# Optimization experiments

Measured on AMD Instinct MI355X. Metric: run time of the kernel, lower is better.

Reference implementation:

```python
import jax, jax.numpy as jnp
import numpy as np

H = 256      # hidden_dim
NH = 8       # num_heads
D = H // NH  # per-head dim
NEG = -(2.0**32) + 1.0
EPS = 1e-5


def setup_inputs() -> dict:
    key = jax.random.key(0)
    ks = jax.random.split(key, 12)
    N, Tq, Tk = 2, 2048, 2048
    s = 1.0 / np.sqrt(H)
    return {
        "Q": jax.random.normal(ks[0], (N, Tq, H), jnp.float32),
        "K": jax.random.normal(ks[1], (N, Tk, H), jnp.float32),
        "V": jax.random.normal(ks[2], (N, Tk, H), jnp.float32),
        "Wq": jax.random.normal(ks[3], (H, H), jnp.float32) * s,
        "bq": jnp.zeros((H,), jnp.float32),
        "Wk": jax.random.normal(ks[4], (H, H), jnp.float32) * s,
        "bk": jnp.zeros((H,), jnp.float32),
        "Wv": jax.random.normal(ks[5], (H, H), jnp.float32) * s,
        "bv": jnp.zeros((H,), jnp.float32),
        "gamma": jnp.ones((H,), jnp.float32),
        "beta": jnp.zeros((H,), jnp.float32),
    }


def _split_heads(x):
    # [N,T,H] -> [h,N,T,D]  (matches torch split(dim=2)+cat(dim=0): head-major)
    N, T, _ = x.shape
    return x.reshape(N, T, NH, D).transpose(2, 0, 1, 3)


def reference(Q, K, V, Wq, bq, Wk, bk, Wv, bv, gamma, beta):
    N, Tq, _ = Q.shape
    Tk = K.shape[1]
    Ql = jax.nn.relu(Q @ Wq + bq)
    Kl = jax.nn.relu(K @ Wk + bk)
    Vl = jax.nn.relu(V @ Wv + bv)
    Qh, Kh, Vh = _split_heads(Ql), _split_heads(Kl), _split_heads(Vl)

    scores = jnp.einsum("hnqd,hnkd->hnqk", Qh, Kh) / jnp.sqrt(jnp.float32(D))
    key_mask = jnp.sign(jnp.abs(K).sum(-1))    # [N,Tk]
    scores = jnp.where(key_mask[None, :, None, :] == 0, NEG, scores)
    attn = jax.nn.softmax(scores / 0.01, axis=-1)
    query_mask = jnp.sign(jnp.abs(Q).sum(-1))  # [N,Tq]
    attn = attn * query_mask[None, :, :, None]  # dropout p=0 -> identity

    ctx = jnp.einsum("hnqk,hnkd->hnqd", attn[..., :-1], Vh[:, :, :-1, :])
    out = ctx.transpose(1, 2, 0, 3).reshape(N, Tq, H)

    mu = out.mean(-1, keepdims=True)
    var = ((out - mu) ** 2).mean(-1, keepdims=True)
    out = (out - mu) / jnp.sqrt(var + EPS) * gamma + beta

    weight = attn.transpose(1, 2, 0, 3).reshape(N, Tq, NH * Tk).mean(-1)
    return out, weight
```

## Files before the change

kernel.cpp:

```cpp
#include <hip/hip_runtime.h>
#include <math.h>

#define H_DIM 256
#define NHEAD 8
#define DHEAD 32
#define NB 2
#define TSEQ 2048
#define LN_EPS 1e-5f

#define QK2_SCALE 25.503486f
#define SPLIT 4
#define TILES_PER (TSEQ / 64 / SPLIT)

typedef _Float16 half8 __attribute__((ext_vector_type(8)));
typedef _Float16 half4t __attribute__((ext_vector_type(4)));
typedef _Float16 half2t __attribute__((ext_vector_type(2)));
typedef float f32x4 __attribute__((ext_vector_type(4)));

__device__ __forceinline__ f32x4 mfma16(half8 a, half8 b, f32x4 c) {
  return __builtin_amdgcn_mfma_f32_16x16x32_f16(a, b, c, 0, 0, 0);
}
__device__ __forceinline__ float exp2fast(float x) {
  return __builtin_amdgcn_exp2f(x);
}
__device__ __forceinline__ half2t pkrtz(float a, float b) {
  return __builtin_bit_cast(half2t, __builtin_amdgcn_cvt_pkrtz(a, b));
}

#define GLOAD_LDS(gp, lp)                                            \
  __builtin_amdgcn_global_load_lds(                                  \
      (const __attribute__((address_space(1))) void*)(gp),           \
      (__attribute__((address_space(3))) void*)(lp), 16, 0, 0)

__global__ __launch_bounds__(256) void pack_mask_kernel(
    const float* __restrict__ K,
    const float* __restrict__ Wq, const float* __restrict__ Wk, const float* __restrict__ Wv,
    float* __restrict__ kmask,
    half8* __restrict__ WpkHi, half8* __restrict__ WpkLo) {
  const int tid = threadIdx.x;
  if (blockIdx.x < 1024) {
    const int wid = tid >> 6, lane = tid & 63;
    int row = blockIdx.x * 4 + wid;
    const float* src = K + (size_t)row * H_DIM;
    float4 v = *(const float4*)(src + lane * 4);
    float s = fabsf(v.x) + fabsf(v.y) + fabsf(v.z) + fabsf(v.w);
    #pragma unroll
    for (int off = 32; off > 0; off >>= 1) s += __shfl_xor(s, off);
    if (lane == 0) kmask[row] = (s != 0.0f) ? 1.0f : 0.0f;
    return;
  }
  int slot = (blockIdx.x - 1024) * 256 + tid;
  int lane = slot & 63;
  int fg = (slot >> 6) & 15;
  int s  = (slot >> 10) & 7;
  int which = slot >> 13;
  const float* W = which == 0 ? Wq : which == 1 ? Wk : Wv;
  int j  = fg * 16 + (lane & 15);
  int kb = s * 32 + (lane >> 4) * 8;
  half8 hi, lo;
  #pragma unroll
  for (int jj = 0; jj < 8; ++jj) {
    float x = W[(size_t)(kb + jj) * H_DIM + j];
    _Float16 h = (_Float16)x;
    hi[jj] = h;
    lo[jj] = (_Float16)(x - (float)h);
  }
  WpkHi[slot] = hi;
  WpkLo[slot] = lo;
}

__global__ __launch_bounds__(256, 3) void proj_kernel(
    const float* __restrict__ Q, const float* __restrict__ K, const float* __restrict__ V,
    const float* __restrict__ bq, const float* __restrict__ bk, const float* __restrict__ bv,
    const half8* __restrict__ WpkHi, const half8* __restrict__ WpkLo,
    const float* __restrict__ kmask,
    half8* __restrict__ Gqhi, half8* __restrict__ Gqlo,
    half8* __restrict__ Gkhi, half8* __restrict__ Gklo, half8* __restrict__ Gv,
    half8* __restrict__ AmaskF, float* __restrict__ qmask) {
  const int which = blockIdx.z;
  const float* X    = which == 0 ? Q  : which == 1 ? K  : V;
  const float* bias = which == 0 ? bq : which == 1 ? bk : bv;

  __shared__ __align__(16) float T[64 * 68];

  const int tid = threadIdx.x;
  const int w = tid >> 6, lane = tid & 63;
  const int l15 = lane & 15, quad = lane >> 4;
  const int mbase = blockIdx.y * 64;
  const int nfg   = blockIdx.x * 4;
  const int nn   = mbase >> 11;
  const int tile = blockIdx.y & 31;

  half8 ahi[8], alo[8];
  {
    const bool doqm = (which == 0) && (blockIdx.x == 0);
    float sabs = 0.0f;
    const float* xrow = X + (size_t)(mbase + w * 16 + l15) * H_DIM + quad * 8;
    #pragma unroll
    for (int s = 0; s < 8; ++s) {
      float4 a0 = *(const float4*)(xrow + s * 32);
      float4 a1 = *(const float4*)(xrow + s * 32 + 4);
      float xs[8] = {a0.x, a0.y, a0.z, a0.w, a1.x, a1.y, a1.z, a1.w};
      if (doqm) {
        #pragma unroll
        for (int i = 0; i < 8; ++i) sabs += fabsf(xs[i]);
      }
      #pragma unroll
      for (int i = 0; i < 8; ++i) {
        _Float16 h = (_Float16)xs[i];
        ahi[s][i] = h;
        alo[s][i] = (_Float16)(xs[i] - (float)h);
      }
    }
    if (doqm) {
      sabs += __shfl_xor(sabs, 16);
      sabs += __shfl_xor(sabs, 32);
      if (quad == 0) qmask[mbase + w * 16 + l15] = (sabs != 0.0f) ? 1.0f : 0.0f;
    }
  }

  f32x4 acc[4];
  #pragma unroll
  for (int f = 0; f < 4; ++f) acc[f] = (f32x4){0.f, 0.f, 0.f, 0.f};

  #pragma unroll
  for (int s = 0; s < 8; ++s) {
    const half8* ph = WpkHi + (((size_t)which * 8 + s) * 16 + nfg) * 64 + lane;
    const half8* pl = WpkLo + (((size_t)which * 8 + s) * 16 + nfg) * 64 + lane;
    #pragma unroll
    for (int f = 0; f < 4; ++f) {
      half8 BH = ph[f * 64];
      half8 BL = pl[f * 64];
      acc[f] = mfma16(ahi[s], BH, acc[f]);
      acc[f] = mfma16(ahi[s], BL, acc[f]);
      acc[f] = mfma16(alo[s], BH, acc[f]);
    }
  }

  #pragma unroll
  for (int f = 0; f < 4; ++f) {
    float bj = bias[blockIdx.x * 64 + f * 16 + l15];
    #pragma unroll
    for (int r = 0; r < 4; ++r) {
      int row = w * 16 + quad * 4 + r;
      float val = fmaxf(acc[f][r] + bj, 0.0f);
      if (which == 2 && ((mbase + row) & (TSEQ - 1)) == TSEQ - 1) val = 0.0f;
      T[row * 68 + f * 16 + l15] = val;
    }
  }
  __syncthreads();

  if (which < 2) {
    const int fq = tid >> 6, lp = tid & 63;
    const int kdc = lp >> 4, krlo = lp & 15;
    const int row = fq * 16 + krlo;
    const float sc = (which == 0) ? QK2_SCALE : 1.0f;
    #pragma unroll
    for (int hs = 0; hs < 2; ++hs) {
      const float* p = &T[row * 68 + hs * 32 + kdc * 8];
      float4 a0 = *(const float4*)p;
      float4 a1 = *(const float4*)(p + 4);
      float xs[8] = {a0.x, a0.y, a0.z, a0.w, a1.x, a1.y, a1.z, a1.w};
      half8 hi, lo;
      #pragma unroll
      for (int i = 0; i < 8; ++i) {
        float x = xs[i] * sc;
        _Float16 h = (_Float16)x;
        hi[i] = h;
        lo[i] = (_Float16)(x - (float)h);
      }
      int hn = (blockIdx.x * 2 + hs) * NB + nn;
      size_t di = ((size_t)hn * 32 + tile) * 256 + tid;
      if (which == 0) { Gqhi[di] = hi; Gqlo[di] = lo; }
      else            { Gkhi[di] = hi; Gklo[di] = lo; }
    }
    if (which == 1 && blockIdx.x == 0 && tid < 128) {
      int c = tid >> 6, lane2 = tid & 63;
      int quad2 = lane2 >> 4, l15b = lane2 & 15;
      half8 am;
      #pragma unroll
      for (int j = 0; j < 8; ++j)
        am[j] = (l15b == 0) ? (_Float16)kmask[(size_t)nn * TSEQ + tile * 64 + c * 32 + quad2 * 8 + j]
                            : (_Float16)0.0f;
      AmaskF[(((size_t)nn * 32 + tile) * 2 + c) * 64 + lane2] = am;
    }
  } else {
    const int top = tid >> 6, mid = (tid >> 4) & 3, low = tid & 15;
    const int c = top >> 1, hh = top & 1;
    const int trow0 = (c * 4 + mid) * 8;
    float km[8];
    #pragma unroll
    for (int j = 0; j < 8; ++j)
      km[j] = kmask[(size_t)nn * TSEQ + tile * 64 + trow0 + j];
    #pragma unroll
    for (int hs = 0; hs < 2; ++hs) {
      const int col = hs * 32 + hh * 16 + low;
      half8 v8;
      #pragma unroll
      for (int j = 0; j < 8; ++j)
        v8[j] = (_Float16)(T[(trow0 + j) * 68 + col] * km[j]);
      int hn = (blockIdx.x * 2 + hs) * NB + nn;
      Gv[((size_t)hn * 32 + tile) * 256 + tid] = v8;
    }
  }
}

__global__ __launch_bounds__(256, 4) void attn_kernel(
    const half8* __restrict__ Gqhi, const half8* __restrict__ Gqlo,
    const half8* __restrict__ Gkhi, const half8* __restrict__ Gklo,
    const half8* __restrict__ Gv, const half8* __restrict__ AmaskF,
    _Float16* __restrict__ Opf, float* __restrict__ Mp, float* __restrict__ Lp) {
  __shared__ __align__(16) half8 KhB[2][256];
  __shared__ __align__(16) half8 KlB[2][256];
  __shared__ __align__(16) half8 VB[2][256];
  __shared__ __align__(16) half8 AB[2][128];
  __shared__ __align__(16) _Float16 Pbuf[4][16][72];

  const int tid = threadIdx.x;
  const int w = tid >> 6, lane = tid & 63;
  const int l15 = lane & 15, quad = lane >> 4;

  const int b = blockIdx.x;
  const int g    = ((b & 7) << 1) | ((b >> 3) & 1);
  const int qt   = (b >> 4) & 15;
  const int sblk = b >> 8;
  const int n = g & 1;

  const size_t fbase = (size_t)g * 32 * 256;
  const int tile0 = sblk * TILES_PER;

  const size_t qoff = fbase + (size_t)(qt * 2) * 256 + w * 64 + lane;
  half8 qhiA = Gqhi[qoff];
  half8 qloA = Gqlo[qoff];
  half8 qhiB = Gqhi[qoff + 256];
  half8 qloB = Gqlo[qoff + 256];

  float mA = -1.0e30f, mB = -1.0e30f;
  f32x4 O0A = {0.f,0.f,0.f,0.f}, O1A = O0A, OlA = O0A;
  f32x4 O0B = O0A, O1B = O0A, OlB = O0A;

  const half8* gkh = Gkhi + fbase + (size_t)tile0 * 256;
  const half8* gkl = Gklo + fbase + (size_t)tile0 * 256;
  const half8* gvv = Gv   + fbase + (size_t)tile0 * 256;
  const half8* gam = AmaskF + (size_t)(n * 32 + tile0) * 128;

  GLOAD_LDS(gkh + tid, &KhB[0][tid]);
  GLOAD_LDS(gkl + tid, &KlB[0][tid]);
  GLOAD_LDS(gvv + tid, &VB[0][tid]);
  if (tid < 128) GLOAD_LDS(gam + tid, &AB[0][tid]);
  __syncthreads();

  #pragma unroll
  for (int tt = 0; tt < TILES_PER; ++tt) {
    const int cur = tt & 1, nxt = cur ^ 1;
    if (tt < TILES_PER - 1) {
      GLOAD_LDS(gkh + (tt + 1) * 256 + tid, &KhB[nxt][tid]);
      GLOAD_LDS(gkl + (tt + 1) * 256 + tid, &KlB[nxt][tid]);
      GLOAD_LDS(gvv + (tt + 1) * 256 + tid, &VB[nxt][tid]);
      if (tid < 128) GLOAD_LDS(gam + (tt + 1) * 128 + tid, &AB[nxt][tid]);
    }

    f32x4 SA[4], SB[4];
    #pragma unroll
    for (int f = 0; f < 4; ++f) {
      half8 KH = KhB[cur][f * 64 + lane];
      half8 KL = KlB[cur][f * 64 + lane];
      f32x4 a = (f32x4){0.f, 0.f, 0.f, 0.f};
      a = mfma16(KL, qhiA, a);
      a = mfma16(KH, qloA, a);
      a = mfma16(KH, qhiA, a);
      SA[f] = a;
      f32x4 bb = (f32x4){0.f, 0.f, 0.f, 0.f};
      bb = mfma16(KL, qhiB, bb);
      bb = mfma16(KH, qloB, bb);
      bb = mfma16(KH, qhiB, bb);
      SB[f] = bb;
    }

    half8 am0 = AB[cur][lane];
    half8 am1 = AB[cur][64 + lane];
    const half8* vbuf = (const half8*)VB[cur];

#define SM_PV(S, m_q, O0, O1, Ol)                                              \
    {                                                                          \
      float t0 = fmaxf(fmaxf(S[0][0], S[0][1]), fmaxf(S[0][2], S[0][3]));      \
      float t1 = fmaxf(fmaxf(S[1][0], S[1][1]), fmaxf(S[1][2], S[1][3]));      \
      float t2 = fmaxf(fmaxf(S[2][0], S[2][1]), fmaxf(S[2][2], S[2][3]));      \
      float t3 = fmaxf(fmaxf(S[3][0], S[3][1]), fmaxf(S[3][2], S[3][3]));      \
      float mx = fmaxf(fmaxf(t0, t1), fmaxf(t2, t3));                          \
      mx = fmaxf(mx, __shfl_xor(mx, 16));                                      \
      mx = fmaxf(mx, __shfl_xor(mx, 32));                                      \
      float mnew = fmaxf(m_q, mx);                                             \
      float alpha = exp2fast(m_q - mnew);                                      \
      m_q = mnew;                                                              \
      _Pragma("unroll")                                                        \
      for (int f = 0; f < 4; ++f) {                                            \
        float p0 = exp2fast(S[f][0] - m_q);                                    \
        float p1 = exp2fast(S[f][1] - m_q);                                    \
        float p2 = exp2fast(S[f][2] - m_q);                                    \
        float p3 = exp2fast(S[f][3] - m_q);                                    \
        half2t a01 = pkrtz(p0, p1);                                            \
        half2t a23 = pkrtz(p2, p3);                                            \
        half4t pk4;                                                            \
        pk4[0] = a01[0]; pk4[1] = a01[1]; pk4[2] = a23[0]; pk4[3] = a23[1];    \
        *(half4t*)&Pbuf[w][l15][f * 16 + quad * 4] = pk4;                      \
      }                                                                        \
      _Pragma("unroll")                                                        \
      for (int r = 0; r < 4; ++r) { O0[r] *= alpha; O1[r] *= alpha; }          \
      Ol[0] *= alpha;                                                          \
      asm volatile("s_waitcnt lgkmcnt(0)" ::: "memory");                       \
      _Pragma("unroll")                                                        \
      for (int c = 0; c < 2; ++c) {                                            \
        half8 pb = *(const half8*)&Pbuf[w][l15][c * 32 + quad * 8];            \
        O0 = mfma16(vbuf[(c * 2 + 0) * 64 + lane], pb, O0);                    \
        O1 = mfma16(vbuf[(c * 2 + 1) * 64 + lane], pb, O1);                    \
        Ol = mfma16(c == 0 ? am0 : am1, pb, Ol);                               \
      }                                                                        \
    }

    SM_PV(SA, mA, O0A, O1A, OlA)
    SM_PV(SB, mB, O0B, O1B, OlB)
#undef SM_PV

    __syncthreads();
  }

  {
    int qA = qt * 128 + w * 16 + l15;
    size_t rowbase = (size_t)(sblk * 16 + g) * TSEQ;
    size_t idxA = (rowbase + qA) * DHEAD;
    size_t idxB = (rowbase + qA + 64) * DHEAD;
    half4t o0A = {(_Float16)O0A[0], (_Float16)O0A[1], (_Float16)O0A[2], (_Float16)O0A[3]};
    half4t o1A = {(_Float16)O1A[0], (_Float16)O1A[1], (_Float16)O1A[2], (_Float16)O1A[3]};
    half4t o0B = {(_Float16)O0B[0], (_Float16)O0B[1], (_Float16)O0B[2], (_Float16)O0B[3]};
    half4t o1B = {(_Float16)O1B[0], (_Float16)O1B[1], (_Float16)O1B[2], (_Float16)O1B[3]};
    *(half4t*)&Opf[idxA + quad * 4]      = o0A;
    *(half4t*)&Opf[idxA + 16 + quad * 4] = o1A;
    *(half4t*)&Opf[idxB + quad * 4]      = o0B;
    *(half4t*)&Opf[idxB + 16 + quad * 4] = o1B;
    if (quad == 0) {
      Mp[rowbase + qA]      = mA;
      Lp[rowbase + qA]      = OlA[0];
      Mp[rowbase + qA + 64] = mB;
      Lp[rowbase + qA + 64] = OlB[0];
    }
  }
}

__global__ __launch_bounds__(256) void ln_kernel(
    const _Float16* __restrict__ Opf, const float* __restrict__ Mp, const float* __restrict__ Lp,
    const float* __restrict__ gamma, const float* __restrict__ beta,
    const float* __restrict__ qmask,
    float* __restrict__ out, float* __restrict__ wout) {
  const int wid = threadIdx.x >> 6, lane = threadIdx.x & 63;
  const int row = blockIdx.x * 4 + wid;
  const int n = row >> 11, q = row & (TSEQ - 1);
  const int hh = lane >> 3;
  const int hn = hh * NB + n;
  const int dbase = (lane & 7) * 4;

  float m[SPLIT], l[SPLIT];
  half4t P[SPLIT];
  #pragma unroll
  for (int i = 0; i < SPLIT; ++i) {
    size_t si = (size_t)(i * 16 + hn) * TSEQ + q;
    P[i] = *(const half4t*)&Opf[si * DHEAD + dbase];
    m[i] = Mp[si];
    l[i] = Lp[si];
  }
  float mm = m[0];
  #pragma unroll
  for (int i = 1; i < SPLIT; ++i) mm = fmaxf(mm, m[i]);
  float denom = 0.f;
  float a[SPLIT];
  #pragma unroll
  for (int i = 0; i < SPLIT; ++i) { a[i] = exp2fast(m[i] - mm); denom += l[i] * a[i]; }
  float qm = qmask[row];
  float inv = qm / denom;

  float4 x = make_float4(0.f, 0.f, 0.f, 0.f);
  #pragma unroll
  for (int i = 0; i < SPLIT; ++i) {
    x.x += (float)P[i][0] * a[i]; x.y += (float)P[i][1] * a[i];
    x.z += (float)P[i][2] * a[i]; x.w += (float)P[i][3] * a[i];
  }
  x.x *= inv; x.y *= inv; x.z *= inv; x.w *= inv;

  float s = x.x + x.y + x.z + x.w;
  #pragma unroll
  for (int off = 32; off > 0; off >>= 1) s += __shfl_xor(s, off);
  float mu = s * (1.0f / H_DIM);
  float dx0 = x.x - mu, dx1 = x.y - mu, dx2 = x.z - mu, dx3 = x.w - mu;
  float sq = dx0 * dx0 + dx1 * dx1 + dx2 * dx2 + dx3 * dx3;
  #pragma unroll
  for (int off = 32; off > 0; off >>= 1) sq += __shfl_xor(sq, off);
  float rstd = rsqrtf(sq * (1.0f / H_DIM) + LN_EPS);
  float4 g = *(const float4*)(gamma + lane * 4);
  float4 bb = *(const float4*)(beta + lane * 4);
  float4 y;
  y.x = dx0 * rstd * g.x + bb.x;
  y.y = dx1 * rstd * g.y + bb.y;
  y.z = dx2 * rstd * g.z + bb.z;
  y.w = dx3 * rstd * g.w + bb.w;
  *(float4*)(out + (size_t)row * H_DIM + lane * 4) = y;
  if (lane == 0) wout[row] = qm * (1.0f / TSEQ);
}

extern "C" void kernel_launch(void* const* d_in, const int* in_sizes, int n_in,
                              void* d_out, int out_size, void* d_ws, size_t ws_size,
                              hipStream_t stream) {
  const float* Q  = (const float*)d_in[0];
  const float* K  = (const float*)d_in[1];
  const float* V  = (const float*)d_in[2];
  const float* Wq = (const float*)d_in[3];
  const float* bq = (const float*)d_in[4];
  const float* Wk = (const float*)d_in[5];
  const float* bk = (const float*)d_in[6];
  const float* Wv = (const float*)d_in[7];
  const float* bv = (const float*)d_in[8];
  const float* gamma = (const float*)d_in[9];
  const float* beta  = (const float*)d_in[10];

  char* ws = (char*)d_ws;
  const size_t NFRAG = (size_t)16 * 32 * 256;
  _Float16* Opf = (_Float16*)ws;
  half8* Gqhi = (half8*)(ws + (size_t)SPLIT * 16 * TSEQ * DHEAD * 2);
  half8* Gqlo = Gqhi + NFRAG;
  half8* Gkhi = Gqlo + NFRAG;
  half8* Gklo = Gkhi + NFRAG;
  half8* Gv   = Gklo + NFRAG;
  float* Mp = (float*)(Gv + NFRAG);
  float* Lp = Mp + SPLIT * 16 * TSEQ;
  float* qmask = Lp + SPLIT * 16 * TSEQ;
  float* kmask = qmask + NB * TSEQ;
  half8* WpkHi = (half8*)(kmask + NB * TSEQ);
  half8* WpkLo = WpkHi + 24576;
  half8* AmaskF = WpkLo + 24576;

  float* out  = (float*)d_out;
  float* wout = out + (size_t)NB * TSEQ * H_DIM;

  hipLaunchKernelGGL(pack_mask_kernel, dim3(1024 + 96), dim3(256), 0, stream,
                     K, Wq, Wk, Wv, kmask, WpkHi, WpkLo);
  hipLaunchKernelGGL(proj_kernel, dim3(H_DIM / 64, NB * TSEQ / 64, 3), dim3(256), 0, stream,
                     Q, K, V, bq, bk, bv, WpkHi, WpkLo, kmask,
                     Gqhi, Gqlo, Gkhi, Gklo, Gv, AmaskF, qmask);
  hipLaunchKernelGGL(attn_kernel, dim3(16 * 16 * SPLIT), dim3(256), 0, stream,
                     Gqhi, Gqlo, Gkhi, Gklo, Gv, AmaskF, Opf, Mp, Lp);
  hipLaunchKernelGGL(ln_kernel, dim3(NB * TSEQ / 4), dim3(256), 0, stream,
                     Opf, Mp, Lp, gamma, beta, qmask, out, wout);
}
```

Before: 124.4 us.

## Remove pack/mask kernel; split weights inline and apply key mask in attention

Drops the separate weight-packing and key-mask kernel. The projection kernel now reads fp32 weights directly and splits them into fp16 hi/lo parts on the fly, and it computes the key mask alongside the query mask. The attention kernel loads a per-tile fp32 key mask into shared memory and multiplies it into the softmax probabilities, replacing the precomputed mask fragments with a constant ones vector for the row-sum. This saves one launch and the intermediate buffers. In exchange, the projection kernel does strided scalar weight loads and repeated conversions in every block, and the attention inner loop gains extra multiplies and shared-memory reads.

```diff
diff --git a/kernel.cpp b/kernel.cpp
--- a/kernel.cpp
+++ b/kernel.cpp
@@ -32,53 +32,16 @@
       (const __attribute__((address_space(1))) void*)(gp),           \
       (__attribute__((address_space(3))) void*)(lp), 16, 0, 0)
 
-__global__ __launch_bounds__(256) void pack_mask_kernel(
-    const float* __restrict__ K,
-    const float* __restrict__ Wq, const float* __restrict__ Wk, const float* __restrict__ Wv,
-    float* __restrict__ kmask,
-    half8* __restrict__ WpkHi, half8* __restrict__ WpkLo) {
-  const int tid = threadIdx.x;
-  if (blockIdx.x < 1024) {
-    const int wid = tid >> 6, lane = tid & 63;
-    int row = blockIdx.x * 4 + wid;
-    const float* src = K + (size_t)row * H_DIM;
-    float4 v = *(const float4*)(src + lane * 4);
-    float s = fabsf(v.x) + fabsf(v.y) + fabsf(v.z) + fabsf(v.w);
-    #pragma unroll
-    for (int off = 32; off > 0; off >>= 1) s += __shfl_xor(s, off);
-    if (lane == 0) kmask[row] = (s != 0.0f) ? 1.0f : 0.0f;
-    return;
-  }
-  int slot = (blockIdx.x - 1024) * 256 + tid;
-  int lane = slot & 63;
-  int fg = (slot >> 6) & 15;
-  int s  = (slot >> 10) & 7;
-  int which = slot >> 13;
-  const float* W = which == 0 ? Wq : which == 1 ? Wk : Wv;
-  int j  = fg * 16 + (lane & 15);
-  int kb = s * 32 + (lane >> 4) * 8;
-  half8 hi, lo;
-  #pragma unroll
-  for (int jj = 0; jj < 8; ++jj) {
-    float x = W[(size_t)(kb + jj) * H_DIM + j];
-    _Float16 h = (_Float16)x;
-    hi[jj] = h;
-    lo[jj] = (_Float16)(x - (float)h);
-  }
-  WpkHi[slot] = hi;
-  WpkLo[slot] = lo;
-}
-
 __global__ __launch_bounds__(256, 3) void proj_kernel(
     const float* __restrict__ Q, const float* __restrict__ K, const float* __restrict__ V,
+    const float* __restrict__ Wq, const float* __restrict__ Wk, const float* __restrict__ Wv,
     const float* __restrict__ bq, const float* __restrict__ bk, const float* __restrict__ bv,
-    const half8* __restrict__ WpkHi, const half8* __restrict__ WpkLo,
-    const float* __restrict__ kmask,
     half8* __restrict__ Gqhi, half8* __restrict__ Gqlo,
     half8* __restrict__ Gkhi, half8* __restrict__ Gklo, half8* __restrict__ Gv,
-    half8* __restrict__ AmaskF, float* __restrict__ qmask) {
+    float* __restrict__ qmask, float* __restrict__ kmask) {
   const int which = blockIdx.z;
   const float* X    = which == 0 ? Q  : which == 1 ? K  : V;
+  const float* Wsel = which == 0 ? Wq : which == 1 ? Wk : Wv;
   const float* bias = which == 0 ? bq : which == 1 ? bk : bv;
 
   __shared__ __align__(16) float T[64 * 68];
@@ -93,7 +56,7 @@
 
   half8 ahi[8], alo[8];
   {
-    const bool doqm = (which == 0) && (blockIdx.x == 0);
+    const bool domask = (blockIdx.x == 0) && (which < 2);
     float sabs = 0.0f;
     const float* xrow = X + (size_t)(mbase + w * 16 + l15) * H_DIM + quad * 8;
     #pragma unroll
@@ -101,7 +64,7 @@
       float4 a0 = *(const float4*)(xrow + s * 32);
       float4 a1 = *(const float4*)(xrow + s * 32 + 4);
       float xs[8] = {a0.x, a0.y, a0.z, a0.w, a1.x, a1.y, a1.z, a1.w};
-      if (doqm) {
+      if (domask) {
         #pragma unroll
         for (int i = 0; i < 8; ++i) sabs += fabsf(xs[i]);
       }
@@ -112,10 +75,11 @@
         alo[s][i] = (_Float16)(xs[i] - (float)h);
       }
     }
-    if (doqm) {
+    if (domask) {
       sabs += __shfl_xor(sabs, 16);
       sabs += __shfl_xor(sabs, 32);
-      if (quad == 0) qmask[mbase + w * 16 + l15] = (sabs != 0.0f) ? 1.0f : 0.0f;
+      float* dst = (which == 0) ? qmask : kmask;
+      if (quad == 0) dst[mbase + w * 16 + l15] = (sabs != 0.0f) ? 1.0f : 0.0f;
     }
   }
 
@@ -125,12 +89,17 @@
 
   #pragma unroll
   for (int s = 0; s < 8; ++s) {
-    const half8* ph = WpkHi + (((size_t)which * 8 + s) * 16 + nfg) * 64 + lane;
-    const half8* pl = WpkLo + (((size_t)which * 8 + s) * 16 + nfg) * 64 + lane;
     #pragma unroll
     for (int f = 0; f < 4; ++f) {
-      half8 BH = ph[f * 64];
-      half8 BL = pl[f * 64];
+      const float* wp = Wsel + (size_t)(s * 32 + quad * 8) * H_DIM + (nfg + f) * 16 + l15;
+      half8 BH, BL;
+      #pragma unroll
+      for (int jj = 0; jj < 8; ++jj) {
+        float x = wp[(size_t)jj * H_DIM];
+        _Float16 h = (_Float16)x;
+        BH[jj] = h;
+        BL[jj] = (_Float16)(x - (float)h);
+      }
       acc[f] = mfma16(ahi[s], BH, acc[f]);
       acc[f] = mfma16(ahi[s], BL, acc[f]);
       acc[f] = mfma16(alo[s], BH, acc[f]);
@@ -174,31 +143,17 @@
       if (which == 0) { Gqhi[di] = hi; Gqlo[di] = lo; }
       else            { Gkhi[di] = hi; Gklo[di] = lo; }
     }
-    if (which == 1 && blockIdx.x == 0 && tid < 128) {
-      int c = tid >> 6, lane2 = tid & 63;
-      int quad2 = lane2 >> 4, l15b = lane2 & 15;
-      half8 am;
-      #pragma unroll
-      for (int j = 0; j < 8; ++j)
-        am[j] = (l15b == 0) ? (_Float16)kmask[(size_t)nn * TSEQ + tile * 64 + c * 32 + quad2 * 8 + j]
-                            : (_Float16)0.0f;
-      AmaskF[(((size_t)nn * 32 + tile) * 2 + c) * 64 + lane2] = am;
-    }
   } else {
     const int top = tid >> 6, mid = (tid >> 4) & 3, low = tid & 15;
     const int c = top >> 1, hh = top & 1;
     const int trow0 = (c * 4 + mid) * 8;
-    float km[8];
-    #pragma unroll
-    for (int j = 0; j < 8; ++j)
-      km[j] = kmask[(size_t)nn * TSEQ + tile * 64 + trow0 + j];
     #pragma unroll
     for (int hs = 0; hs < 2; ++hs) {
       const int col = hs * 32 + hh * 16 + low;
       half8 v8;
       #pragma unroll
       for (int j = 0; j < 8; ++j)
-        v8[j] = (_Float16)(T[(trow0 + j) * 68 + col] * km[j]);
+        v8[j] = (_Float16)T[(trow0 + j) * 68 + col];
       int hn = (blockIdx.x * 2 + hs) * NB + nn;
       Gv[((size_t)hn * 32 + tile) * 256 + tid] = v8;
     }
@@ -208,12 +163,12 @@
 __global__ __launch_bounds__(256, 4) void attn_kernel(
     const half8* __restrict__ Gqhi, const half8* __restrict__ Gqlo,
     const half8* __restrict__ Gkhi, const half8* __restrict__ Gklo,
-    const half8* __restrict__ Gv, const half8* __restrict__ AmaskF,
+    const half8* __restrict__ Gv, const float* __restrict__ kmask,
     _Float16* __restrict__ Opf, float* __restrict__ Mp, float* __restrict__ Lp) {
   __shared__ __align__(16) half8 KhB[2][256];
   __shared__ __align__(16) half8 KlB[2][256];
   __shared__ __align__(16) half8 VB[2][256];
-  __shared__ __align__(16) half8 AB[2][128];
+  __shared__ __align__(16) float kmS[2][64];
   __shared__ __align__(16) _Float16 Pbuf[4][16][72];
 
   const int tid = threadIdx.x;
@@ -235,6 +190,10 @@
   half8 qhiB = Gqhi[qoff + 256];
   half8 qloB = Gqlo[qoff + 256];
 
+  half8 amONE;
+  #pragma unroll
+  for (int j = 0; j < 8; ++j) amONE[j] = (l15 == 0) ? (_Float16)1.0f : (_Float16)0.0f;
+
   float mA = -1.0e30f, mB = -1.0e30f;
   f32x4 O0A = {0.f,0.f,0.f,0.f}, O1A = O0A, OlA = O0A;
   f32x4 O0B = O0A, O1B = O0A, OlB = O0A;
@@ -242,12 +201,12 @@
   const half8* gkh = Gkhi + fbase + (size_t)tile0 * 256;
   const half8* gkl = Gklo + fbase + (size_t)tile0 * 256;
   const half8* gvv = Gv   + fbase + (size_t)tile0 * 256;
-  const half8* gam = AmaskF + (size_t)(n * 32 + tile0) * 128;
+  const float* kmg = kmask + (size_t)n * TSEQ + tile0 * 64;
 
   GLOAD_LDS(gkh + tid, &KhB[0][tid]);
   GLOAD_LDS(gkl + tid, &KlB[0][tid]);
   GLOAD_LDS(gvv + tid, &VB[0][tid]);
-  if (tid < 128) GLOAD_LDS(gam + tid, &AB[0][tid]);
+  if (tid < 16) GLOAD_LDS(kmg + tid * 4, &kmS[0][tid * 4]);
   __syncthreads();
 
   #pragma unroll
@@ -257,7 +216,7 @@
       GLOAD_LDS(gkh + (tt + 1) * 256 + tid, &KhB[nxt][tid]);
       GLOAD_LDS(gkl + (tt + 1) * 256 + tid, &KlB[nxt][tid]);
       GLOAD_LDS(gvv + (tt + 1) * 256 + tid, &VB[nxt][tid]);
-      if (tid < 128) GLOAD_LDS(gam + (tt + 1) * 128 + tid, &AB[nxt][tid]);
+      if (tid < 16) GLOAD_LDS(kmg + (tt + 1) * 64 + tid * 4, &kmS[nxt][tid * 4]);
     }
 
     f32x4 SA[4], SB[4];
@@ -277,9 +236,8 @@
       SB[f] = bb;
     }
 
-    half8 am0 = AB[cur][lane];
-    half8 am1 = AB[cur][64 + lane];
     const half8* vbuf = (const half8*)VB[cur];
+    const float* kmP = &kmS[cur][0];
 
 #define SM_PV(S, m_q, O0, O1, Ol)                                              \
     {                                                                          \
@@ -295,10 +253,11 @@
       m_q = mnew;                                                              \
       _Pragma("unroll")                                                        \
       for (int f = 0; f < 4; ++f) {                                            \
-        float p0 = exp2fast(S[f][0] - m_q);                                    \
-        float p1 = exp2fast(S[f][1] - m_q);                                    \
-        float p2 = exp2fast(S[f][2] - m_q);                                    \
-        float p3 = exp2fast(S[f][3] - m_q);                                    \
+        f32x4 kmv = *(const f32x4*)&kmP[f * 16 + quad * 4];                    \
+        float p0 = exp2fast(S[f][0] - m_q) * kmv[0];                           \
+        float p1 = exp2fast(S[f][1] - m_q) * kmv[1];                           \
+        float p2 = exp2fast(S[f][2] - m_q) * kmv[2];                           \
+        float p3 = exp2fast(S[f][3] - m_q) * kmv[3];                           \
         half2t a01 = pkrtz(p0, p1);                                            \
         half2t a23 = pkrtz(p2, p3);                                            \
         half4t pk4;                                                            \
@@ -314,7 +273,7 @@
         half8 pb = *(const half8*)&Pbuf[w][l15][c * 32 + quad * 8];            \
         O0 = mfma16(vbuf[(c * 2 + 0) * 64 + lane], pb, O0);                    \
         O1 = mfma16(vbuf[(c * 2 + 1) * 64 + lane], pb, O1);                    \
-        Ol = mfma16(c == 0 ? am0 : am1, pb, Ol);                               \
+        Ol = mfma16(amONE, pb, Ol);                                            \
       }                                                                        \
     }
 
@@ -433,20 +392,15 @@
   float* Lp = Mp + SPLIT * 16 * TSEQ;
   float* qmask = Lp + SPLIT * 16 * TSEQ;
   float* kmask = qmask + NB * TSEQ;
-  half8* WpkHi = (half8*)(kmask + NB * TSEQ);
-  half8* WpkLo = WpkHi + 24576;
-  half8* AmaskF = WpkLo + 24576;
 
   float* out  = (float*)d_out;
   float* wout = out + (size_t)NB * TSEQ * H_DIM;
 
-  hipLaunchKernelGGL(pack_mask_kernel, dim3(1024 + 96), dim3(256), 0, stream,
-                     K, Wq, Wk, Wv, kmask, WpkHi, WpkLo);
   hipLaunchKernelGGL(proj_kernel, dim3(H_DIM / 64, NB * TSEQ / 64, 3), dim3(256), 0, stream,
-                     Q, K, V, bq, bk, bv, WpkHi, WpkLo, kmask,
-                     Gqhi, Gqlo, Gkhi, Gklo, Gv, AmaskF, qmask);
+                     Q, K, V, Wq, Wk, Wv, bq, bk, bv,
+                     Gqhi, Gqlo, Gkhi, Gklo, Gv, qmask, kmask);
   hipLaunchKernelGGL(attn_kernel, dim3(16 * 16 * SPLIT), dim3(256), 0, stream,
-                     Gqhi, Gqlo, Gkhi, Gklo, Gv, AmaskF, Opf, Mp, Lp);
+                     Gqhi, Gqlo, Gkhi, Gklo, Gv, kmask, Opf, Mp, Lp);
   hipLaunchKernelGGL(ln_kernel, dim3(NB * TSEQ / 4), dim3(256), 0, stream,
                      Opf, Mp, Lp, gamma, beta, qmask, out, wout);
 }
```

Result: no change. 126.6 us (+1.8%).

## Apply key mask to softmax probabilities in attention and interleave two query halves

Applied to the files above, without the earlier changes.

Drops the precomputed AmaskF fragment buffer and the V-times-mask step from the projection kernel. The attention kernel instead loads 64 float mask values per tile into LDS and multiplies each exp'd score by them, using a constant ones-fragment MFMA to accumulate the row sum. The two softmax/PV halves are interleaved so B's exponentials are computed while A's P buffer reads are in flight, reusing the single Pbuf. This trades projection-side work and global traffic for extra per-element multiplies and an LDS mask read in the hot loop.

```diff
diff --git a/kernel.cpp b/kernel.cpp
--- a/kernel.cpp
+++ b/kernel.cpp
@@ -73,10 +73,9 @@
     const float* __restrict__ Q, const float* __restrict__ K, const float* __restrict__ V,
     const float* __restrict__ bq, const float* __restrict__ bk, const float* __restrict__ bv,
     const half8* __restrict__ WpkHi, const half8* __restrict__ WpkLo,
-    const float* __restrict__ kmask,
     half8* __restrict__ Gqhi, half8* __restrict__ Gqlo,
     half8* __restrict__ Gkhi, half8* __restrict__ Gklo, half8* __restrict__ Gv,
-    half8* __restrict__ AmaskF, float* __restrict__ qmask) {
+    float* __restrict__ qmask) {
   const int which = blockIdx.z;
   const float* X    = which == 0 ? Q  : which == 1 ? K  : V;
   const float* bias = which == 0 ? bq : which == 1 ? bk : bv;
@@ -174,31 +173,17 @@
       if (which == 0) { Gqhi[di] = hi; Gqlo[di] = lo; }
       else            { Gkhi[di] = hi; Gklo[di] = lo; }
     }
-    if (which == 1 && blockIdx.x == 0 && tid < 128) {
-      int c = tid >> 6, lane2 = tid & 63;
-      int quad2 = lane2 >> 4, l15b = lane2 & 15;
-      half8 am;
-      #pragma unroll
-      for (int j = 0; j < 8; ++j)
-        am[j] = (l15b == 0) ? (_Float16)kmask[(size_t)nn * TSEQ + tile * 64 + c * 32 + quad2 * 8 + j]
-                            : (_Float16)0.0f;
-      AmaskF[(((size_t)nn * 32 + tile) * 2 + c) * 64 + lane2] = am;
-    }
   } else {
     const int top = tid >> 6, mid = (tid >> 4) & 3, low = tid & 15;
     const int c = top >> 1, hh = top & 1;
     const int trow0 = (c * 4 + mid) * 8;
-    float km[8];
-    #pragma unroll
-    for (int j = 0; j < 8; ++j)
-      km[j] = kmask[(size_t)nn * TSEQ + tile * 64 + trow0 + j];
     #pragma unroll
     for (int hs = 0; hs < 2; ++hs) {
       const int col = hs * 32 + hh * 16 + low;
       half8 v8;
       #pragma unroll
       for (int j = 0; j < 8; ++j)
-        v8[j] = (_Float16)(T[(trow0 + j) * 68 + col] * km[j]);
+        v8[j] = (_Float16)T[(trow0 + j) * 68 + col];
       int hn = (blockIdx.x * 2 + hs) * NB + nn;
       Gv[((size_t)hn * 32 + tile) * 256 + tid] = v8;
     }
@@ -208,12 +193,12 @@
 __global__ __launch_bounds__(256, 4) void attn_kernel(
     const half8* __restrict__ Gqhi, const half8* __restrict__ Gqlo,
     const half8* __restrict__ Gkhi, const half8* __restrict__ Gklo,
-    const half8* __restrict__ Gv, const half8* __restrict__ AmaskF,
+    const half8* __restrict__ Gv, const float* __restrict__ kmask,
     _Float16* __restrict__ Opf, float* __restrict__ Mp, float* __restrict__ Lp) {
   __shared__ __align__(16) half8 KhB[2][256];
   __shared__ __align__(16) half8 KlB[2][256];
   __shared__ __align__(16) half8 VB[2][256];
-  __shared__ __align__(16) half8 AB[2][128];
+  __shared__ __align__(16) float kmS[2][64];
   __shared__ __align__(16) _Float16 Pbuf[4][16][72];
 
   const int tid = threadIdx.x;
@@ -235,6 +220,10 @@
   half8 qhiB = Gqhi[qoff + 256];
   half8 qloB = Gqlo[qoff + 256];
 
+  half8 amONE;
+  #pragma unroll
+  for (int j = 0; j < 8; ++j) amONE[j] = (l15 == 0) ? (_Float16)1.0f : (_Float16)0.0f;
+
   float mA = -1.0e30f, mB = -1.0e30f;
   f32x4 O0A = {0.f,0.f,0.f,0.f}, O1A = O0A, OlA = O0A;
   f32x4 O0B = O0A, O1B = O0A, OlB = O0A;
@@ -242,12 +231,12 @@
   const half8* gkh = Gkhi + fbase + (size_t)tile0 * 256;
   const half8* gkl = Gklo + fbase + (size_t)tile0 * 256;
   const half8* gvv = Gv   + fbase + (size_t)tile0 * 256;
-  const half8* gam = AmaskF + (size_t)(n * 32 + tile0) * 128;
+  const float* kmg = kmask + (size_t)n * TSEQ + tile0 * 64;
 
   GLOAD_LDS(gkh + tid, &KhB[0][tid]);
   GLOAD_LDS(gkl + tid, &KlB[0][tid]);
   GLOAD_LDS(gvv + tid, &VB[0][tid]);
-  if (tid < 128) GLOAD_LDS(gam + tid, &AB[0][tid]);
+  if (tid < 16) GLOAD_LDS(kmg + tid * 4, &kmS[0][tid * 4]);
   __syncthreads();
 
   #pragma unroll
@@ -257,7 +246,7 @@
       GLOAD_LDS(gkh + (tt + 1) * 256 + tid, &KhB[nxt][tid]);
       GLOAD_LDS(gkl + (tt + 1) * 256 + tid, &KlB[nxt][tid]);
       GLOAD_LDS(gvv + (tt + 1) * 256 + tid, &VB[nxt][tid]);
-      if (tid < 128) GLOAD_LDS(gam + (tt + 1) * 128 + tid, &AB[nxt][tid]);
+      if (tid < 16) GLOAD_LDS(kmg + (tt + 1) * 64 + tid * 4, &kmS[nxt][tid * 4]);
     }
 
     f32x4 SA[4], SB[4];
@@ -277,50 +266,82 @@
       SB[f] = bb;
     }
 
-    half8 am0 = AB[cur][lane];
-    half8 am1 = AB[cur][64 + lane];
     const half8* vbuf = (const half8*)VB[cur];
-
-#define SM_PV(S, m_q, O0, O1, Ol)                                              \
-    {                                                                          \
-      float t0 = fmaxf(fmaxf(S[0][0], S[0][1]), fmaxf(S[0][2], S[0][3]));      \
-      float t1 = fmaxf(fmaxf(S[1][0], S[1][1]), fmaxf(S[1][2], S[1][3]));      \
-      float t2 = fmaxf(fmaxf(S[2][0], S[2][1]), fmaxf(S[2][2], S[2][3]));      \
-      float t3 = fmaxf(fmaxf(S[3][0], S[3][1]), fmaxf(S[3][2], S[3][3]));      \
-      float mx = fmaxf(fmaxf(t0, t1), fmaxf(t2, t3));                          \
-      mx = fmaxf(mx, __shfl_xor(mx, 16));                                      \
-      mx = fmaxf(mx, __shfl_xor(mx, 32));                                      \
-      float mnew = fmaxf(m_q, mx);                                             \
-      float alpha = exp2fast(m_q - mnew);                                      \
-      m_q = mnew;                                                              \
-      _Pragma("unroll")                                                        \
-      for (int f = 0; f < 4; ++f) {                                            \
-        float p0 = exp2fast(S[f][0] - m_q);                                    \
-        float p1 = exp2fast(S[f][1] - m_q);                                    \
-        float p2 = exp2fast(S[f][2] - m_q);                                    \
-        float p3 = exp2fast(S[f][3] - m_q);                                    \
-        half2t a01 = pkrtz(p0, p1);                                            \
-        half2t a23 = pkrtz(p2, p3);                                            \
-        half4t pk4;                                                            \
-        pk4[0] = a01[0]; pk4[1] = a01[1]; pk4[2] = a23[0]; pk4[3] = a23[1];    \
-        *(half4t*)&Pbuf[w][l15][f * 16 + quad * 4] = pk4;                      \
-      }                                                                        \
-      _Pragma("unroll")                                                        \
-      for (int r = 0; r < 4; ++r) { O0[r] *= alpha; O1[r] *= alpha; }          \
-      Ol[0] *= alpha;                                                          \
-      asm volatile("s_waitcnt lgkmcnt(0)" ::: "memory");                       \
-      _Pragma("unroll")                                                        \
-      for (int c = 0; c < 2; ++c) {                                            \
-        half8 pb = *(const half8*)&Pbuf[w][l15][c * 32 + quad * 8];            \
-        O0 = mfma16(vbuf[(c * 2 + 0) * 64 + lane], pb, O0);                    \
-        O1 = mfma16(vbuf[(c * 2 + 1) * 64 + lane], pb, O1);                    \
-        Ol = mfma16(c == 0 ? am0 : am1, pb, Ol);                               \
-      }                                                                        \
-    }
-
-    SM_PV(SA, mA, O0A, O1A, OlA)
-    SM_PV(SB, mB, O0B, O1B, OlB)
-#undef SM_PV
+    const float* kmP = &kmS[cur][0];
+
+    float tA0 = fmaxf(fmaxf(SA[0][0], SA[0][1]), fmaxf(SA[0][2], SA[0][3]));
+    float tA1 = fmaxf(fmaxf(SA[1][0], SA[1][1]), fmaxf(SA[1][2], SA[1][3]));
+    float tA2 = fmaxf(fmaxf(SA[2][0], SA[2][1]), fmaxf(SA[2][2], SA[2][3]));
+    float tA3 = fmaxf(fmaxf(SA[3][0], SA[3][1]), fmaxf(SA[3][2], SA[3][3]));
+    float tB0 = fmaxf(fmaxf(SB[0][0], SB[0][1]), fmaxf(SB[0][2], SB[0][3]));
+    float tB1 = fmaxf(fmaxf(SB[1][0], SB[1][1]), fmaxf(SB[1][2], SB[1][3]));
+    float tB2 = fmaxf(fmaxf(SB[2][0], SB[2][1]), fmaxf(SB[2][2], SB[2][3]));
+    float tB3 = fmaxf(fmaxf(SB[3][0], SB[3][1]), fmaxf(SB[3][2], SB[3][3]));
+    float mxA = fmaxf(fmaxf(tA0, tA1), fmaxf(tA2, tA3));
+    float mxB = fmaxf(fmaxf(tB0, tB1), fmaxf(tB2, tB3));
+    mxA = fmaxf(mxA, __shfl_xor(mxA, 16));
+    mxB = fmaxf(mxB, __shfl_xor(mxB, 16));
+    mxA = fmaxf(mxA, __shfl_xor(mxA, 32));
+    mxB = fmaxf(mxB, __shfl_xor(mxB, 32));
+    float mnA = fmaxf(mA, mxA);
+    float mnB = fmaxf(mB, mxB);
+    float alA = exp2fast(mA - mnA);
+    float alB = exp2fast(mB - mnB);
+    mA = mnA; mB = mnB;
+
+    #pragma unroll
+    for (int f = 0; f < 4; ++f) {
+      f32x4 kmv = *(const f32x4*)&kmP[f * 16 + quad * 4];
+      float p0 = exp2fast(SA[f][0] - mA) * kmv[0];
+      float p1 = exp2fast(SA[f][1] - mA) * kmv[1];
+      float p2 = exp2fast(SA[f][2] - mA) * kmv[2];
+      float p3 = exp2fast(SA[f][3] - mA) * kmv[3];
+      half2t a01 = pkrtz(p0, p1);
+      half2t a23 = pkrtz(p2, p3);
+      half4t pk4;
+      pk4[0] = a01[0]; pk4[1] = a01[1]; pk4[2] = a23[0]; pk4[3] = a23[1];
+      *(half4t*)&Pbuf[w][l15][f * 16 + quad * 4] = pk4;
+    }
+    half4t pkB[4];
+    #pragma unroll
+    for (int f = 0; f < 4; ++f) {
+      f32x4 kmv = *(const f32x4*)&kmP[f * 16 + quad * 4];
+      float p0 = exp2fast(SB[f][0] - mB) * kmv[0];
+      float p1 = exp2fast(SB[f][1] - mB) * kmv[1];
+      float p2 = exp2fast(SB[f][2] - mB) * kmv[2];
+      float p3 = exp2fast(SB[f][3] - mB) * kmv[3];
+      half2t a01 = pkrtz(p0, p1);
+      half2t a23 = pkrtz(p2, p3);
+      pkB[f][0] = a01[0]; pkB[f][1] = a01[1]; pkB[f][2] = a23[0]; pkB[f][3] = a23[1];
+    }
+    #pragma unroll
+    for (int r = 0; r < 4; ++r) { O0A[r] *= alA; O1A[r] *= alA; O0B[r] *= alB; O1B[r] *= alB; }
+    OlA[0] *= alA; OlB[0] *= alB;
+
+    asm volatile("s_waitcnt lgkmcnt(0)" ::: "memory");
+    half8 pbA0 = *(const half8*)&Pbuf[w][l15][0 * 32 + quad * 8];
+    half8 pbA1 = *(const half8*)&Pbuf[w][l15][1 * 32 + quad * 8];
+    #pragma unroll
+    for (int f = 0; f < 4; ++f)
+      *(half4t*)&Pbuf[w][l15][f * 16 + quad * 4] = pkB[f];
+
+    O0A = mfma16(vbuf[0 * 64 + lane], pbA0, O0A);
+    O1A = mfma16(vbuf[1 * 64 + lane], pbA0, O1A);
+    OlA = mfma16(amONE, pbA0, OlA);
+    O0A = mfma16(vbuf[2 * 64 + lane], pbA1, O0A);
+    O1A = mfma16(vbuf[3 * 64 + lane], pbA1, O1A);
+    OlA = mfma16(amONE, pbA1, OlA);
+
+    asm volatile("s_waitcnt lgkmcnt(0)" ::: "memory");
+    half8 pbB0 = *(const half8*)&Pbuf[w][l15][0 * 32 + quad * 8];
+    half8 pbB1 = *(const half8*)&Pbuf[w][l15][1 * 32 + quad * 8];
+
+    O0B = mfma16(vbuf[0 * 64 + lane], pbB0, O0B);
+    O1B = mfma16(vbuf[1 * 64 + lane], pbB0, O1B);
+    OlB = mfma16(amONE, pbB0, OlB);
+    O0B = mfma16(vbuf[2 * 64 + lane], pbB1, O0B);
+    O1B = mfma16(vbuf[3 * 64 + lane], pbB1, O1B);
+    OlB = mfma16(amONE, pbB1, OlB);
 
     __syncthreads();
   }
@@ -435,7 +456,6 @@
   float* kmask = qmask + NB * TSEQ;
   half8* WpkHi = (half8*)(kmask + NB * TSEQ);
   half8* WpkLo = WpkHi + 24576;
-  half8* AmaskF = WpkLo + 24576;
 
   float* out  = (float*)d_out;
   float* wout = out + (size_t)NB * TSEQ * H_DIM;
@@ -443,10 +463,10 @@
   hipLaunchKernelGGL(pack_mask_kernel, dim3(1024 + 96), dim3(256), 0, stream,
                      K, Wq, Wk, Wv, kmask, WpkHi, WpkLo);
   hipLaunchKernelGGL(proj_kernel, dim3(H_DIM / 64, NB * TSEQ / 64, 3), dim3(256), 0, stream,
-                     Q, K, V, bq, bk, bv, WpkHi, WpkLo, kmask,
-                     Gqhi, Gqlo, Gkhi, Gklo, Gv, AmaskF, qmask);
+                     Q, K, V, bq, bk, bv, WpkHi, WpkLo,
+                     Gqhi, Gqlo, Gkhi, Gklo, Gv, qmask);
   hipLaunchKernelGGL(attn_kernel, dim3(16 * 16 * SPLIT), dim3(256), 0, stream,
-                     Gqhi, Gqlo, Gkhi, Gklo, Gv, AmaskF, Opf, Mp, Lp);
+                     Gqhi, Gqlo, Gkhi, Gklo, Gv, kmask, Opf, Mp, Lp);
   hipLaunchKernelGGL(ln_kernel, dim3(NB * TSEQ / 4), dim3(256), 0, stream,
                      Opf, Mp, Lp, gamma, beta, qmask, out, wout);
 }
```

Result: no change. 126.8 us (+2.0%).
